# Performance work log

Hardware: AMD Instinct MI355X
Metric: run time of the kernel (lower is better)

Reference implementation:

```python
import jax, jax.numpy as jnp
import numpy as np

VOCAB, EMBED, HIDDEN, FEAT = 193, 256, 512, 512
MAX_LEN = 15


def setup_inputs() -> dict:
    key = jax.random.key(0)
    ks = jax.random.split(key, 12)
    B = 8192
    s = 0.05  # small init scale for weights
    return {
        "img_feats": jax.random.normal(ks[0], (B, FEAT), jnp.float32),
        "text": jax.random.randint(ks[1], (B, MAX_LEN), 0, VOCAB, jnp.int64),
        "emb": jax.random.uniform(ks[2], (VOCAB, EMBED), jnp.float32, -0.1, 0.1),
        "W_proj": jax.random.normal(ks[3], (HIDDEN, FEAT), jnp.float32) * s,
        "b_proj": jnp.zeros((HIDDEN,), jnp.float32),
        "W_ih": jax.random.normal(ks[4], (3 * HIDDEN, EMBED), jnp.float32) * s,
        "W_hh": jax.random.normal(ks[5], (3 * HIDDEN, HIDDEN), jnp.float32) * s,
        "b_ih": jax.random.normal(ks[6], (3 * HIDDEN,), jnp.float32) * s,
        "b_hh": jax.random.normal(ks[7], (3 * HIDDEN,), jnp.float32) * s,
        "W_out": jax.random.uniform(ks[8], (VOCAB, HIDDEN), jnp.float32, -0.1, 0.1),
        "b_out": jnp.zeros((VOCAB,), jnp.float32),
    }


def reference(img_feats, text, emb, W_proj, b_proj, W_ih, W_hh, b_ih, b_hh, W_out, b_out):
    # h0 = project(img_feats)   [B, H]
    h0 = img_feats @ W_proj.T + b_proj
    # Teacher-forced decoder inputs: tokens text[:, 0..13] -> embeddings [T=14, B, E]
    xs = emb[text[:, : MAX_LEN - 1]].transpose(1, 0, 2)

    def gru_step(h, x):
        gi = x @ W_ih.T + b_ih   # [B, 3H]
        gh = h @ W_hh.T + b_hh   # [B, 3H]
        i_r, i_z, i_n = jnp.split(gi, 3, axis=-1)
        h_r, h_z, h_n = jnp.split(gh, 3, axis=-1)
        r = jax.nn.sigmoid(i_r + h_r)
        z = jax.nn.sigmoid(i_z + h_z)
        n = jnp.tanh(i_n + r * h_n)
        h_new = (1.0 - z) * n + z * h
        return h_new, h_new

    _, hs = jax.lax.scan(gru_step, h0, xs)  # hs: [T, B, H]
    preds = hs @ W_out.T + b_out            # [T, B, V]
    return preds.transpose(1, 0, 2)         # [B, T=14, V]
```

## Files before the change

### kernel.cpp

```cpp
#include <hip/hip_runtime.h>
#include <stdint.h>

using bf16x8 = __attribute__((ext_vector_type(8))) __bf16;
using f32x4  = __attribute__((ext_vector_type(4))) float;

#define AS1 __attribute__((address_space(1)))
#define AS3 __attribute__((address_space(3)))

constexpr size_t OFF_WHH   = 0;
constexpr size_t OFF_WPROJ = OFF_WHH   + (size_t)1536*512*2;
constexpr size_t OFF_WOUT  = OFF_WPROJ + (size_t)512*512*2;
constexpr size_t OFF_WIH   = OFF_WOUT  + (size_t)256*512*2;
constexpr size_t OFF_EMBBF = OFF_WIH   + (size_t)1536*256*2;
constexpr size_t OFF_BHN   = OFF_EMBBF + (size_t)256*256*2;
constexpr size_t OFF_BPROJ = OFF_BHN   + 2048;
constexpr size_t OFF_BOUT  = OFF_BPROJ + 2048;
constexpr size_t OFF_BCAT  = OFF_BOUT  + 1024;
constexpr size_t OFF_EP    = OFF_BCAT  + 1536*4;
constexpr size_t OFF_HS    = OFF_EP    + (size_t)193*512*16;
constexpr size_t OFF_IMG   = OFF_HS    + (size_t)15*8192*512*2;
constexpr size_t WS_NEED   = OFF_IMG   + (size_t)8192*512*2;

constexpr size_t SLAB = (size_t)8192 * 512;

__device__ __forceinline__ short f2bf(float f) {
  union { float f; unsigned u; } v; v.f = f;
  unsigned u = v.u;
  u += 0x7FFFu + ((u >> 16) & 1u);
  return (short)(u >> 16);
}
__device__ __forceinline__ float bf2f(short s) {
  union { float f; unsigned u; } v; v.u = ((unsigned)(unsigned short)s) << 16;
  return v.f;
}
__device__ __forceinline__ float sigm(float x) { return 1.f / (1.f + __expf(-x)); }
__device__ __forceinline__ float tanh_fast(float x) {
  x = fminf(fmaxf(x, -15.f), 15.f);
  float e = __expf(-2.f * x);
  return (1.f - e) / (1.f + e);
}

template<int ROWS, int WAVES>
__device__ __forceinline__ void stage_tile(const short* __restrict__ src, size_t row0,
                                           int stride, int k0, char* lds, int tid) {
  const int w = tid >> 6;
  const int lane = tid & 63;
#pragma unroll
  for (int s = 0; s < ROWS / (8 * WAVES); ++s) {
    const int rowbase = s * (8 * WAVES) + w * 8;
    const int row = rowbase + (lane >> 3);
    const int colE = ((lane & 7) ^ (row & 7)) * 8;
    const short* g = src + (row0 + (size_t)row) * (size_t)stride + k0 + colE;
    __builtin_amdgcn_global_load_lds((const AS1 int*)g, (AS3 int*)(lds + rowbase * 128),
                                     16, 0, 0);
  }
}

__device__ __forceinline__ bf16x8 read_frag(const char* lds, int row, int ks, int lane) {
  const int kb = ks * 64 + ((lane >> 4) << 4);
  return *(const bf16x8*)(lds + row * 128 + (kb ^ ((row & 7) << 4)));
}

__global__ void prep_kernel(const float* __restrict__ W_proj, const float* __restrict__ b_proj,
                            const float* __restrict__ W_hh, const float* __restrict__ b_hh,
                            const float* __restrict__ W_ih, const float* __restrict__ b_ih,
                            const float* __restrict__ emb,
                            const float* __restrict__ W_out, const float* __restrict__ b_out,
                            short* __restrict__ whh, short* __restrict__ wproj,
                            short* __restrict__ wout, short* __restrict__ wih,
                            short* __restrict__ embbf,
                            float* __restrict__ bhn, float* __restrict__ bproj,
                            float* __restrict__ bout, float* __restrict__ bcat) {
  const int total = 1536*512 + 512*512 + 256*512 + 1536*256 + 256*256 + 512 + 512 + 256 + 1536;
  const int stride = gridDim.x * blockDim.x;
  for (int i = blockIdx.x * blockDim.x + threadIdx.x; i < total; i += stride) {
    int j = i;
    if (j < 1536*512) { whh[j] = f2bf(W_hh[j]); continue; }
    j -= 1536*512;
    if (j < 512*512) { wproj[j] = f2bf(W_proj[j]); continue; }
    j -= 512*512;
    if (j < 256*512) {
      int r = j / 512, c = j % 512;
      wout[j] = f2bf(r < 193 ? W_out[r*512 + c] : 0.f);
      continue;
    }
    j -= 256*512;
    if (j < 1536*256) { wih[j] = f2bf(W_ih[j]); continue; }
    j -= 1536*256;
    if (j < 256*256) {
      int r = j >> 8, c = j & 255;
      embbf[j] = f2bf(r < 193 ? emb[r*256 + c] : 0.f);
      continue;
    }
    j -= 256*256;
    if (j < 512) { bhn[j] = b_hh[1024 + j]; continue; }
    j -= 512;
    if (j < 512) { bproj[j] = b_proj[j]; continue; }
    j -= 512;
    if (j < 256) { bout[j] = (j < 193) ? b_out[j] : 0.f; continue; }
    j -= 256;
    bcat[j] = b_ih[j] + (j < 1024 ? b_hh[j] : 0.f);
  }
}

__global__ void imgcvt_kernel(const float* __restrict__ img, short* __restrict__ imgbf) {
  const int i = blockIdx.x * blockDim.x + threadIdx.x;
  const float4 v = *(const float4*)(img + (size_t)i * 4);
  short4 o; o.x = f2bf(v.x); o.y = f2bf(v.y); o.z = f2bf(v.z); o.w = f2bf(v.w);
  *(short4*)(imgbf + (size_t)i * 4) = o;
}

__global__ __launch_bounds__(256, 4)
void embproj_mfma_kernel(const short* __restrict__ embbf, const short* __restrict__ wih,
                         const float* __restrict__ bcat, float* __restrict__ ep) {
  __shared__ __align__(16) char smem[40960];
  char* ldsA = smem;
  char* ldsB = smem + 8192;
  const int tid = threadIdx.x;
  const int lane = tid & 63;
  const int w = tid >> 6;
  const int wr = w >> 1, wc = w & 1;
  const unsigned m0 = blockIdx.x * 64;
  const int j0 = blockIdx.y * 256;

  f32x4 acc[2][8];
#pragma unroll
  for (int a = 0; a < 2; ++a)
#pragma unroll
    for (int b = 0; b < 8; ++b) acc[a][b] = f32x4{0.f, 0.f, 0.f, 0.f};

  for (int it = 0; it < 4; ++it) {
    const int k0 = it * 64;
    __syncthreads();
    stage_tile<64, 4>(embbf, m0, 256, k0, ldsA, tid);
    stage_tile<256, 4>(wih, (size_t)j0, 256, k0, ldsB, tid);
    __syncthreads();
#pragma unroll
    for (int ks = 0; ks < 2; ++ks) {
      bf16x8 af[2];
#pragma unroll
      for (int mi = 0; mi < 2; ++mi)
        af[mi] = read_frag(ldsA, wr*32 + mi*16 + (lane & 15), ks, lane);
#pragma unroll
      for (int ji = 0; ji < 8; ++ji) {
        bf16x8 bfm = read_frag(ldsB, wc*128 + ji*16 + (lane & 15), ks, lane);
#pragma unroll
        for (int mi = 0; mi < 2; ++mi)
          acc[mi][ji] = __builtin_amdgcn_mfma_f32_16x16x32_bf16(af[mi], bfm, acc[mi][ji], 0, 0, 0);
      }
    }
  }
#pragma unroll
  for (int ji = 0; ji < 8; ++ji) {
    const int c = j0 + wc*128 + ji*16 + (lane & 15);
    const int gate = c >> 9, jj = c & 511;
    const float bc = bcat[c];
#pragma unroll
    for (int mi = 0; mi < 2; ++mi) {
#pragma unroll
      for (int i = 0; i < 4; ++i) {
        const unsigned v = m0 + wr*32 + mi*16 + ((lane >> 4) * 4) + i;
        if (v < 193) ep[((size_t)v * 512 + jj) * 4 + gate] = acc[mi][ji][i] + bc;
      }
    }
  }
}

template<int MODE>
__global__ __launch_bounds__(256, 4)
void gemm_kernel(const short* __restrict__ A, const short* __restrict__ Bw,
                 const float* __restrict__ bias, float* __restrict__ out_f,
                 short* __restrict__ out_bf) {
  __shared__ __align__(16) char smem[40960];
  char* ldsA = smem;
  char* ldsB = smem + 8192;
  const int tid = threadIdx.x;
  const int lane = tid & 63;
  const int w = tid >> 6;
  const int wr = w >> 1, wc = w & 1;
  const unsigned m0 = blockIdx.x * 64;
  const int j0 = blockIdx.y * 256;

  f32x4 acc[2][8];
#pragma unroll
  for (int a = 0; a < 2; ++a)
#pragma unroll
    for (int b = 0; b < 8; ++b) acc[a][b] = f32x4{0.f, 0.f, 0.f, 0.f};

  for (int it = 0; it < 8; ++it) {
    const int k0 = it * 64;
    __syncthreads();
    if (MODE == 0) {
      stage_tile<64, 4>(A, m0, 512, k0, ldsA, tid);
    } else {
#pragma unroll
      for (int s = 0; s < 2; ++s) {
        const int rowbase = s * 32 + w * 8;
        const int row = rowbase + (lane >> 3);
        const unsigned m = m0 + row;
        const unsigned b = m / 14u, t = m - b * 14u;
        const int colE = ((lane & 7) ^ (row & 7)) * 8;
        const short* g = A + ((size_t)t * 8192 + b) * 512 + k0 + colE;
        __builtin_amdgcn_global_load_lds((const AS1 int*)g, (AS3 int*)(ldsA + rowbase * 128),
                                         16, 0, 0);
      }
    }
    stage_tile<256, 4>(Bw, (size_t)j0, 512, k0, ldsB, tid);
    __syncthreads();
#pragma unroll
    for (int ks = 0; ks < 2; ++ks) {
      bf16x8 af[2];
#pragma unroll
      for (int mi = 0; mi < 2; ++mi)
        af[mi] = read_frag(ldsA, wr*32 + mi*16 + (lane & 15), ks, lane);
#pragma unroll
      for (int ji = 0; ji < 8; ++ji) {
        bf16x8 bfm = read_frag(ldsB, wc*128 + ji*16 + (lane & 15), ks, lane);
#pragma unroll
        for (int mi = 0; mi < 2; ++mi)
          acc[mi][ji] = __builtin_amdgcn_mfma_f32_16x16x32_bf16(af[mi], bfm, acc[mi][ji], 0, 0, 0);
      }
    }
  }
#pragma unroll
  for (int ji = 0; ji < 8; ++ji) {
    const int j = j0 + wc*128 + ji*16 + (lane & 15);
    const float bj = bias[j];
#pragma unroll
    for (int mi = 0; mi < 2; ++mi) {
#pragma unroll
      for (int i = 0; i < 4; ++i) {
        const size_t m = m0 + wr*32 + mi*16 + ((lane >> 4) * 4) + i;
        const float v = acc[mi][ji][i] + bj;
        if (MODE == 0) {
          out_bf[m * 512 + j] = f2bf(v);
        } else {
          if (j < 193) out_f[m * 193 + j] = v;
        }
      }
    }
  }
}

__global__ __launch_bounds__(256, 2)
void gate_kernel(const short* __restrict__ Hbf, const short* __restrict__ whh,
                 const int* __restrict__ text, const int t,
                 const float4* __restrict__ ep4, const float* __restrict__ bhn,
                 short* __restrict__ hs_out) {
  __shared__ __align__(16) char smem[81920];
  char* ldsA0 = smem;
  char* ldsA1 = smem + 16384;
  char* ldsB0 = smem + 32768;
  char* ldsB1 = smem + 57344;
  const int tid = threadIdx.x;
  const int lane = tid & 63;
  const int w = tid >> 6;
  const int wr = w >> 1, wc = w & 1;
  const unsigned raw = blockIdx.x;
  const unsigned xcd = raw & 7, slot = raw >> 3;
  const unsigned mt = xcd * 8 + (slot & 7), jt = slot >> 3;
  const size_t m0 = (size_t)mt * 128;
  const int j0 = jt * 64;

  int toks[4][4];
#pragma unroll
  for (int mi = 0; mi < 4; ++mi)
#pragma unroll
    for (int i = 0; i < 4; ++i) {
      const size_t m = m0 + wr*64 + mi*16 + ((lane >> 4) * 4) + i;
      toks[mi][i] = text[m * 15 + t];
    }

  f32x4 acc_r[4][2], acc_z[4][2], acc_hn[4][2];
#pragma unroll
  for (int a = 0; a < 4; ++a)
#pragma unroll
    for (int b = 0; b < 2; ++b) {
      acc_r[a][b] = f32x4{0.f, 0.f, 0.f, 0.f};
      acc_z[a][b] = f32x4{0.f, 0.f, 0.f, 0.f};
      acc_hn[a][b] = f32x4{0.f, 0.f, 0.f, 0.f};
    }

  for (int it = 0; it < 4; ++it) {
    const int k0 = it * 128;
    __syncthreads();
    stage_tile<128, 4>(Hbf, m0, 512, k0, ldsA0, tid);
    stage_tile<128, 4>(Hbf, m0, 512, k0 + 64, ldsA1, tid);
#pragma unroll
    for (int g = 0; g < 3; ++g) {
      stage_tile<64, 4>(whh, (size_t)(g * 512 + j0), 512, k0,      ldsB0 + g * 8192, tid);
      stage_tile<64, 4>(whh, (size_t)(g * 512 + j0), 512, k0 + 64, ldsB1 + g * 8192, tid);
    }
    __syncthreads();
#pragma unroll
    for (int half = 0; half < 2; ++half) {
      const char* lA = half ? ldsA1 : ldsA0;
      const char* lB = half ? ldsB1 : ldsB0;
#pragma unroll
      for (int ks = 0; ks < 2; ++ks) {
        bf16x8 af[4];
#pragma unroll
        for (int mi = 0; mi < 4; ++mi)
          af[mi] = read_frag(lA, wr*64 + mi*16 + (lane & 15), ks, lane);
#pragma unroll
        for (int ji = 0; ji < 2; ++ji) {
          const int nb = wc*32 + ji*16 + (lane & 15);
          bf16x8 b_r = read_frag(lB,         nb, ks, lane);
          bf16x8 b_z = read_frag(lB + 8192,  nb, ks, lane);
          bf16x8 b_n = read_frag(lB + 16384, nb, ks, lane);
#pragma unroll
          for (int mi = 0; mi < 4; ++mi) {
            acc_r[mi][ji]  = __builtin_amdgcn_mfma_f32_16x16x32_bf16(af[mi], b_r, acc_r[mi][ji], 0, 0, 0);
            acc_z[mi][ji]  = __builtin_amdgcn_mfma_f32_16x16x32_bf16(af[mi], b_z, acc_z[mi][ji], 0, 0, 0);
            acc_hn[mi][ji] = __builtin_amdgcn_mfma_f32_16x16x32_bf16(af[mi], b_n, acc_hn[mi][ji], 0, 0, 0);
          }
        }
      }
    }
  }
#pragma unroll
  for (int ji = 0; ji < 2; ++ji) {
    const int j = j0 + wc*32 + ji*16 + (lane & 15);
    const float vbhn = bhn[j];
#pragma unroll
    for (int mi = 0; mi < 4; ++mi) {
#pragma unroll
      for (int i = 0; i < 4; ++i) {
        const size_t m = m0 + wr*64 + mi*16 + ((lane >> 4) * 4) + i;
        const float4 e = ep4[(size_t)toks[mi][i] * 512 + j];
        const float r = sigm(acc_r[mi][ji][i] + e.x);
        const float z = sigm(acc_z[mi][ji][i] + e.y);
        const float n = tanh_fast(e.z + r * (acc_hn[mi][ji][i] + vbhn));
        const float hold = bf2f(Hbf[m * 512 + j]);
        hs_out[m * 512 + j] = f2bf((1.f - z) * n + z * hold);
      }
    }
  }
}

extern "C" void kernel_launch(void* const* d_in, const int* in_sizes, int n_in,
                              void* d_out, int out_size, void* d_ws, size_t ws_size,
                              hipStream_t stream) {
  (void)in_sizes; (void)n_in; (void)out_size;
  if (ws_size < WS_NEED) return;

  const float* img    = (const float*)d_in[0];
  const int*   text   = (const int*)  d_in[1];
  const float* emb    = (const float*)d_in[2];
  const float* W_proj = (const float*)d_in[3];
  const float* b_proj = (const float*)d_in[4];
  const float* W_ih   = (const float*)d_in[5];
  const float* W_hh   = (const float*)d_in[6];
  const float* b_ih   = (const float*)d_in[7];
  const float* b_hh   = (const float*)d_in[8];
  const float* W_out  = (const float*)d_in[9];
  const float* b_out  = (const float*)d_in[10];
  float* out = (float*)d_out;
  char* ws = (char*)d_ws;

  short* whh   = (short*)(ws + OFF_WHH);
  short* wproj = (short*)(ws + OFF_WPROJ);
  short* wout  = (short*)(ws + OFF_WOUT);
  short* wih   = (short*)(ws + OFF_WIH);
  short* embbf = (short*)(ws + OFF_EMBBF);
  float* bhn   = (float*)(ws + OFF_BHN);
  float* bproj = (float*)(ws + OFF_BPROJ);
  float* bout  = (float*)(ws + OFF_BOUT);
  float* bcat  = (float*)(ws + OFF_BCAT);
  float* epf   = (float*)(ws + OFF_EP);
  float4* ep4  = (float4*)(ws + OFF_EP);
  short* hs    = (short*)(ws + OFF_HS);
  short* imgbf = (short*)(ws + OFF_IMG);

  prep_kernel<<<512, 256, 0, stream>>>(W_proj, b_proj, W_hh, b_hh, W_ih, b_ih, emb,
                                       W_out, b_out,
                                       whh, wproj, wout, wih, embbf,
                                       bhn, bproj, bout, bcat);
  imgcvt_kernel<<<4096, 256, 0, stream>>>(img, imgbf);

  embproj_mfma_kernel<<<dim3(4, 6), 256, 0, stream>>>(embbf, wih, bcat, epf);

  gemm_kernel<0><<<dim3(128, 2), 256, 0, stream>>>(imgbf, wproj, bproj, nullptr, hs);

  for (int t = 0; t < 14; ++t) {
    const short* Hb = hs + (size_t)t * SLAB;
    short* Ho       = hs + (size_t)(t + 1) * SLAB;
    gate_kernel<<<512, 256, 0, stream>>>(Hb, whh, text, t, ep4, bhn, Ho);
  }

  gemm_kernel<1><<<dim3(1792, 1), 256, 0, stream>>>(hs + (size_t)8192 * 512, wout, bout,
                                                    out, nullptr);
}
```

Before: 378.5 us.

## Use 512-thread blocks for gate and output GEMMs with smaller per-wave tiles

The gate kernel moves from 256 to 512 threads per block. Each wave now handles 32 rows instead of 64, and the k-loop runs single-buffered in 64-wide steps with half the LDS, which should raise occupancy and latency hiding. The output GEMM becomes a dedicated kernel with 128-row tiles and 8 waves, halving the grid size and staging W_out once per k-step for twice as many rows. The trade-off is more barriers per step, and the output GEMM's 256-column tile still wastes compute on padding past 193.

```diff
diff --git a/kernel.cpp b/kernel.cpp
--- a/kernel.cpp
+++ b/kernel.cpp
@@ -166,11 +166,9 @@
   }
 }
 
-template<int MODE>
 __global__ __launch_bounds__(256, 4)
-void gemm_kernel(const short* __restrict__ A, const short* __restrict__ Bw,
-                 const float* __restrict__ bias, float* __restrict__ out_f,
-                 short* __restrict__ out_bf) {
+void h0_kernel(const short* __restrict__ A, const short* __restrict__ Bw,
+               const float* __restrict__ bias, short* __restrict__ out_bf) {
   __shared__ __align__(16) char smem[40960];
   char* ldsA = smem;
   char* ldsB = smem + 8192;
@@ -190,21 +188,7 @@
   for (int it = 0; it < 8; ++it) {
     const int k0 = it * 64;
     __syncthreads();
-    if (MODE == 0) {
-      stage_tile<64, 4>(A, m0, 512, k0, ldsA, tid);
-    } else {
-#pragma unroll
-      for (int s = 0; s < 2; ++s) {
-        const int rowbase = s * 32 + w * 8;
-        const int row = rowbase + (lane >> 3);
-        const unsigned m = m0 + row;
-        const unsigned b = m / 14u, t = m - b * 14u;
-        const int colE = ((lane & 7) ^ (row & 7)) * 8;
-        const short* g = A + ((size_t)t * 8192 + b) * 512 + k0 + colE;
-        __builtin_amdgcn_global_load_lds((const AS1 int*)g, (AS3 int*)(ldsA + rowbase * 128),
-                                         16, 0, 0);
-      }
-    }
+    stage_tile<64, 4>(A, m0, 512, k0, ldsA, tid);
     stage_tile<256, 4>(Bw, (size_t)j0, 512, k0, ldsB, tid);
     __syncthreads();
 #pragma unroll
@@ -231,27 +215,84 @@
 #pragma unroll
       for (int i = 0; i < 4; ++i) {
         const size_t m = m0 + wr*32 + mi*16 + ((lane >> 4) * 4) + i;
-        const float v = acc[mi][ji][i] + bj;
-        if (MODE == 0) {
-          out_bf[m * 512 + j] = f2bf(v);
-        } else {
-          if (j < 193) out_f[m * 193 + j] = v;
-        }
-      }
-    }
-  }
-}
-
-__global__ __launch_bounds__(256, 2)
+        out_bf[m * 512 + j] = f2bf(acc[mi][ji][i] + bj);
+      }
+    }
+  }
+}
+
+__global__ __launch_bounds__(512, 2)
+void out_gemm_kernel(const short* __restrict__ A, const short* __restrict__ Bw,
+                     const float* __restrict__ bias, float* __restrict__ out_f) {
+  __shared__ __align__(16) char smem[49152];
+  char* ldsA = smem;
+  char* ldsB = smem + 16384;
+  const int tid = threadIdx.x;
+  const int lane = tid & 63;
+  const int w = tid >> 6;
+  const int wr = w >> 2, wc = w & 3;
+  const unsigned m0 = blockIdx.x * 128;
+
+  f32x4 acc[4][4];
+#pragma unroll
+  for (int a = 0; a < 4; ++a)
+#pragma unroll
+    for (int b = 0; b < 4; ++b) acc[a][b] = f32x4{0.f, 0.f, 0.f, 0.f};
+
+  for (int it = 0; it < 8; ++it) {
+    const int k0 = it * 64;
+    __syncthreads();
+#pragma unroll
+    for (int s = 0; s < 2; ++s) {
+      const int rowbase = s * 64 + w * 8;
+      const int row = rowbase + (lane >> 3);
+      const unsigned m = m0 + row;
+      const unsigned b = m / 14u, t = m - b * 14u;
+      const int colE = ((lane & 7) ^ (row & 7)) * 8;
+      const short* g = A + ((size_t)t * 8192 + b) * 512 + k0 + colE;
+      __builtin_amdgcn_global_load_lds((const AS1 int*)g, (AS3 int*)(ldsA + rowbase * 128),
+                                       16, 0, 0);
+    }
+    stage_tile<256, 8>(Bw, 0, 512, k0, ldsB, tid);
+    __syncthreads();
+#pragma unroll
+    for (int ks = 0; ks < 2; ++ks) {
+      bf16x8 af[4];
+#pragma unroll
+      for (int mi = 0; mi < 4; ++mi)
+        af[mi] = read_frag(ldsA, wr*64 + mi*16 + (lane & 15), ks, lane);
+#pragma unroll
+      for (int ji = 0; ji < 4; ++ji) {
+        bf16x8 bfm = read_frag(ldsB, wc*64 + ji*16 + (lane & 15), ks, lane);
+#pragma unroll
+        for (int mi = 0; mi < 4; ++mi)
+          acc[mi][ji] = __builtin_amdgcn_mfma_f32_16x16x32_bf16(af[mi], bfm, acc[mi][ji], 0, 0, 0);
+      }
+    }
+  }
+#pragma unroll
+  for (int ji = 0; ji < 4; ++ji) {
+    const int j = wc*64 + ji*16 + (lane & 15);
+    const float bj = bias[j];
+#pragma unroll
+    for (int mi = 0; mi < 4; ++mi) {
+#pragma unroll
+      for (int i = 0; i < 4; ++i) {
+        const size_t m = m0 + wr*64 + mi*16 + ((lane >> 4) * 4) + i;
+        if (j < 193) out_f[m * 193 + j] = acc[mi][ji][i] + bj;
+      }
+    }
+  }
+}
+
+__global__ __launch_bounds__(512, 2)
 void gate_kernel(const short* __restrict__ Hbf, const short* __restrict__ whh,
                  const int* __restrict__ text, const int t,
                  const float4* __restrict__ ep4, const float* __restrict__ bhn,
                  short* __restrict__ hs_out) {
-  __shared__ __align__(16) char smem[81920];
-  char* ldsA0 = smem;
-  char* ldsA1 = smem + 16384;
-  char* ldsB0 = smem + 32768;
-  char* ldsB1 = smem + 57344;
+  __shared__ __align__(16) char smem[40960];
+  char* ldsA = smem;
+  char* ldsB = smem + 16384;
   const int tid = threadIdx.x;
   const int lane = tid & 63;
   const int w = tid >> 6;
@@ -262,18 +303,18 @@
   const size_t m0 = (size_t)mt * 128;
   const int j0 = jt * 64;
 
-  int toks[4][4];
-#pragma unroll
-  for (int mi = 0; mi < 4; ++mi)
+  int toks[2][4];
+#pragma unroll
+  for (int mi = 0; mi < 2; ++mi)
 #pragma unroll
     for (int i = 0; i < 4; ++i) {
-      const size_t m = m0 + wr*64 + mi*16 + ((lane >> 4) * 4) + i;
+      const size_t m = m0 + wr*32 + mi*16 + ((lane >> 4) * 4) + i;
       toks[mi][i] = text[m * 15 + t];
     }
 
-  f32x4 acc_r[4][2], acc_z[4][2], acc_hn[4][2];
-#pragma unroll
-  for (int a = 0; a < 4; ++a)
+  f32x4 acc_r[2][2], acc_z[2][2], acc_hn[2][2];
+#pragma unroll
+  for (int a = 0; a < 2; ++a)
 #pragma unroll
     for (int b = 0; b < 2; ++b) {
       acc_r[a][b] = f32x4{0.f, 0.f, 0.f, 0.f};
@@ -281,39 +322,31 @@
       acc_hn[a][b] = f32x4{0.f, 0.f, 0.f, 0.f};
     }
 
-  for (int it = 0; it < 4; ++it) {
-    const int k0 = it * 128;
-    __syncthreads();
-    stage_tile<128, 4>(Hbf, m0, 512, k0, ldsA0, tid);
-    stage_tile<128, 4>(Hbf, m0, 512, k0 + 64, ldsA1, tid);
-#pragma unroll
-    for (int g = 0; g < 3; ++g) {
-      stage_tile<64, 4>(whh, (size_t)(g * 512 + j0), 512, k0,      ldsB0 + g * 8192, tid);
-      stage_tile<64, 4>(whh, (size_t)(g * 512 + j0), 512, k0 + 64, ldsB1 + g * 8192, tid);
-    }
-    __syncthreads();
-#pragma unroll
-    for (int half = 0; half < 2; ++half) {
-      const char* lA = half ? ldsA1 : ldsA0;
-      const char* lB = half ? ldsB1 : ldsB0;
-#pragma unroll
-      for (int ks = 0; ks < 2; ++ks) {
-        bf16x8 af[4];
-#pragma unroll
-        for (int mi = 0; mi < 4; ++mi)
-          af[mi] = read_frag(lA, wr*64 + mi*16 + (lane & 15), ks, lane);
-#pragma unroll
-        for (int ji = 0; ji < 2; ++ji) {
-          const int nb = wc*32 + ji*16 + (lane & 15);
-          bf16x8 b_r = read_frag(lB,         nb, ks, lane);
-          bf16x8 b_z = read_frag(lB + 8192,  nb, ks, lane);
-          bf16x8 b_n = read_frag(lB + 16384, nb, ks, lane);
-#pragma unroll
-          for (int mi = 0; mi < 4; ++mi) {
-            acc_r[mi][ji]  = __builtin_amdgcn_mfma_f32_16x16x32_bf16(af[mi], b_r, acc_r[mi][ji], 0, 0, 0);
-            acc_z[mi][ji]  = __builtin_amdgcn_mfma_f32_16x16x32_bf16(af[mi], b_z, acc_z[mi][ji], 0, 0, 0);
-            acc_hn[mi][ji] = __builtin_amdgcn_mfma_f32_16x16x32_bf16(af[mi], b_n, acc_hn[mi][ji], 0, 0, 0);
-          }
+  for (int it = 0; it < 8; ++it) {
+    const int k0 = it * 64;
+    __syncthreads();
+    stage_tile<128, 8>(Hbf, m0, 512, k0, ldsA, tid);
+#pragma unroll
+    for (int g = 0; g < 3; ++g)
+      stage_tile<64, 8>(whh, (size_t)(g * 512 + j0), 512, k0, ldsB + g * 8192, tid);
+    __syncthreads();
+#pragma unroll
+    for (int ks = 0; ks < 2; ++ks) {
+      bf16x8 af[2];
+#pragma unroll
+      for (int mi = 0; mi < 2; ++mi)
+        af[mi] = read_frag(ldsA, wr*32 + mi*16 + (lane & 15), ks, lane);
+#pragma unroll
+      for (int ji = 0; ji < 2; ++ji) {
+        const int nb = wc*32 + ji*16 + (lane & 15);
+        bf16x8 b_r = read_frag(ldsB,         nb, ks, lane);
+        bf16x8 b_z = read_frag(ldsB + 8192,  nb, ks, lane);
+        bf16x8 b_n = read_frag(ldsB + 16384, nb, ks, lane);
+#pragma unroll
+        for (int mi = 0; mi < 2; ++mi) {
+          acc_r[mi][ji]  = __builtin_amdgcn_mfma_f32_16x16x32_bf16(af[mi], b_r, acc_r[mi][ji], 0, 0, 0);
+          acc_z[mi][ji]  = __builtin_amdgcn_mfma_f32_16x16x32_bf16(af[mi], b_z, acc_z[mi][ji], 0, 0, 0);
+          acc_hn[mi][ji] = __builtin_amdgcn_mfma_f32_16x16x32_bf16(af[mi], b_n, acc_hn[mi][ji], 0, 0, 0);
         }
       }
     }
@@ -323,10 +356,10 @@
     const int j = j0 + wc*32 + ji*16 + (lane & 15);
     const float vbhn = bhn[j];
 #pragma unroll
-    for (int mi = 0; mi < 4; ++mi) {
+    for (int mi = 0; mi < 2; ++mi) {
 #pragma unroll
       for (int i = 0; i < 4; ++i) {
-        const size_t m = m0 + wr*64 + mi*16 + ((lane >> 4) * 4) + i;
+        const size_t m = m0 + wr*32 + mi*16 + ((lane >> 4) * 4) + i;
         const float4 e = ep4[(size_t)toks[mi][i] * 512 + j];
         const float r = sigm(acc_r[mi][ji][i] + e.x);
         const float z = sigm(acc_z[mi][ji][i] + e.y);
@@ -380,14 +413,14 @@
 
   embproj_mfma_kernel<<<dim3(4, 6), 256, 0, stream>>>(embbf, wih, bcat, epf);
 
-  gemm_kernel<0><<<dim3(128, 2), 256, 0, stream>>>(imgbf, wproj, bproj, nullptr, hs);
+  h0_kernel<<<dim3(128, 2), 256, 0, stream>>>(imgbf, wproj, bproj, hs);
 
   for (int t = 0; t < 14; ++t) {
     const short* Hb = hs + (size_t)t * SLAB;
     short* Ho       = hs + (size_t)(t + 1) * SLAB;
-    gate_kernel<<<512, 256, 0, stream>>>(Hb, whh, text, t, ep4, bhn, Ho);
-  }
-
-  gemm_kernel<1><<<dim3(1792, 1), 256, 0, stream>>>(hs + (size_t)8192 * 512, wout, bout,
-                                                    out, nullptr);
-}
+    gate_kernel<<<512, 512, 0, stream>>>(Hb, whh, text, t, ep4, bhn, Ho);
+  }
+
+  out_gemm_kernel<<<dim3(896, 1), 512, 0, stream>>>(hs + (size_t)8192 * 512, wout, bout,
+                                                    out);
+}
```

Result: slower. 474.1 us (+25.2%).
